# Optimization experiments

Hardware: AMD Instinct MI355X
Metric: run time of the kernel (lower is better)

The kernel has to match this reference:

```python
import jax, jax.numpy as jnp
import numpy as np

N, H, M, B = 512, 64, 1024, 256
ETA = 1.0
INIT_STD = 0.01

def setup_inputs() -> dict:
    key = jax.random.key(0)
    k1, k2, k3, k4 = jax.random.split(key, 4)
    # Binary +/-1 sequences and memory (as produced upstream in the repo)
    sequences = jnp.where(jax.random.uniform(k1, (B, N)) < 0.5, -1.0, 1.0).astype(jnp.float32)
    memory = jnp.where(jax.random.uniform(k2, (M, N)) < 0.5, -1.0, 1.0).astype(jnp.float32)
    A_logits = (INIT_STD * jax.random.normal(k3, (N, H, N))).astype(jnp.float32)
    B_logits = (INIT_STD * jax.random.normal(k4, (H, N))).astype(jnp.float32)
    return {"sequences": sequences, "memory": memory, "A_logits": A_logits, "B_logits": B_logits}

def reference(sequences, memory, A_logits, B_logits):
    # Vectorized version of DAM.train_batch's loss over positions n=1..N-1.
    n_dim = sequences.shape[1]
    # Causal mask: row for position n attends to indices i < n. Rows n=1..N-1.
    ns = jnp.arange(1, n_dim)[:, None, None]            # (N-1,1,1)
    idx = jnp.arange(n_dim)[None, None, :]              # (1,1,N)
    mask = idx < ns                                      # (N-1,1,N)
    neg_inf = jnp.asarray(-jnp.inf, A_logits.dtype)
    A = jax.nn.softmax(jnp.where(mask, A_logits[1:], neg_inf), axis=-1)  # (N-1,H,N), zeros outside mask
    Bn = jax.nn.softmax(B_logits, axis=-1)               # (H,N)
    phi_mu = jnp.einsum('hn,mn->mh', Bn, memory)         # (M,H) memory keys
    hat_phi = jnp.einsum('bi,nhi->bnh', sequences, A)    # (B,N-1,H) queries for every position at once
    score = ETA * jnp.einsum('bnh,mh->bnm', hat_phi, phi_mu)  # (B,N-1,M)
    pi = jax.nn.softmax(score, axis=-1)                  # retrieval distribution over memories
    plus = (memory[:, 1:] > 0).astype(pi.dtype)          # (M,N-1): memory bit at position n is +1
    prob = jnp.einsum('bnm,mn->bn', pi, plus)            # P(next bit = +1)
    prob = jnp.clip(prob, 1e-6, 1.0 - 1e-6)
    target = (sequences[:, 1:] > 0).astype(prob.dtype)
    bce = -(target * jnp.log(prob) + (1.0 - target) * jnp.log1p(-prob))
    # mean over batch per position, summed over positions, / (N-1) == global mean
    return jnp.mean(bce)
```

## Files before the change

kernel.cpp:

```cpp
#include <hip/hip_runtime.h>
#include <stdint.h>

#define NPOS 512
#define NH   64
#define NM   1024
#define NB   256
#define NM1  511

typedef __attribute__((ext_vector_type(8)))  short bf16x8;
typedef __attribute__((ext_vector_type(16))) float f32x16;
typedef __attribute__((ext_vector_type(4)))  float f32x4;
typedef __attribute__((ext_vector_type(4)))  int   i32x4;

#if __has_builtin(__builtin_amdgcn_exp2f)
#define EXP2F(x) __builtin_amdgcn_exp2f(x)
#else
#define EXP2F(x) __expf((x) * 0.69314718055994531f)
#endif

__device__ __forceinline__ unsigned short f2bf(float x) {
    unsigned u = __float_as_uint(x);
    u = (u + 0x7FFFu + ((u >> 16) & 1u)) >> 16;
    return (unsigned short)u;
}
__device__ __forceinline__ int pack2(unsigned short a, unsigned short b) {
    return (int)a | ((int)b << 16);
}

__global__ __launch_bounds__(256, 4)
void kA_prep(const float* __restrict__ seq, const float* __restrict__ Bl,
             const float* __restrict__ mem,
             unsigned short* __restrict__ seq_bf, float* __restrict__ BnT,
             float* __restrict__ plusT, float* __restrict__ out) {
    const int bid = blockIdx.x, t = threadIdx.x;
    if (bid < 128) {
        if (bid == 0 && t == 0) out[0] = 0.f;
        int idx = (bid * 256 + t) * 4;
        f32x4 v = *(const f32x4*)(seq + idx);
        int2 o;
        o.x = pack2(f2bf(v.x), f2bf(v.y));
        o.y = pack2(f2bf(v.z), f2bf(v.w));
        *(int2*)(seq_bf + idx) = o;
    } else if (bid < 144) {
        const int h = (bid - 128) * 4 + (t >> 6), l = t & 63;
        float v[8]; float mx = -1e30f;
#pragma unroll
        for (int j = 0; j < 8; j++) { v[j] = Bl[h * NPOS + l + 64 * j]; mx = fmaxf(mx, v[j]); }
#pragma unroll
        for (int o = 32; o; o >>= 1) mx = fmaxf(mx, __shfl_xor(mx, o));
        float s = 0.f;
#pragma unroll
        for (int j = 0; j < 8; j++) { v[j] = __expf(v[j] - mx); s += v[j]; }
#pragma unroll
        for (int o = 32; o; o >>= 1) s += __shfl_xor(s, o);
        float r = 1.0f / s;
#pragma unroll
        for (int j = 0; j < 8; j++) BnT[(l + 64 * j) * NH + h] = v[j] * r;
    } else {
        __shared__ float sT[64][65];
        const int bb = bid - 144;
        const int mt = bb >> 3, nt = bb & 7;
        const int rr = t >> 2, cc = t & 3;
        const float* src = mem + (size_t)(mt * 64 + rr) * NPOS + nt * 64 + cc * 16;
#pragma unroll
        for (int j = 0; j < 4; j++) {
            f32x4 v = *(const f32x4*)(src + j * 4);
            sT[rr][cc * 16 + j * 4 + 0] = (v.x > 0.f) ? 1.f : 0.f;
            sT[rr][cc * 16 + j * 4 + 1] = (v.y > 0.f) ? 1.f : 0.f;
            sT[rr][cc * 16 + j * 4 + 2] = (v.z > 0.f) ? 1.f : 0.f;
            sT[rr][cc * 16 + j * 4 + 3] = (v.w > 0.f) ? 1.f : 0.f;
        }
        __syncthreads();
        float* dst = plusT + (size_t)(nt * 64 + rr) * NM + mt * 64 + cc * 16;
#pragma unroll
        for (int j = 0; j < 4; j++) {
            f32x4 o;
            o.x = sT[cc * 16 + j * 4 + 0][rr];
            o.y = sT[cc * 16 + j * 4 + 1][rr];
            o.z = sT[cc * 16 + j * 4 + 2][rr];
            o.w = sT[cc * 16 + j * 4 + 3][rr];
            *(f32x4*)(dst + j * 4) = o;
        }
    }
}

__global__ __launch_bounds__(256, 4)
void k1b_phimu(const float* __restrict__ BnT, const float* __restrict__ mem,
               unsigned short* __restrict__ phimu) {
    const int m0 = blockIdx.x * 2, t = threadIdx.x;
    __shared__ float mrow[2][NPOS];
    __shared__ float part[2][256];
    {
        int row = t >> 7, c = (t & 127) * 4;
        *(f32x4*)(&mrow[row][c]) = *(const f32x4*)(mem + (size_t)(m0 + row) * NPOS + c);
    }
    __syncthreads();
    const int h = t & 63, seg = t >> 6;
    float a[2] = {0.f, 0.f};
    float b2[2] = {0.f, 0.f};
    const float* bp = BnT + seg * 128 * NH + h;
#pragma unroll 8
    for (int nn = 0; nn < 128; nn += 2) {
        float x0 = bp[nn * NH], x1 = bp[(nn + 1) * NH];
#pragma unroll
        for (int row = 0; row < 2; row++) {
            a[row]  = fmaf(x0, mrow[row][seg * 128 + nn], a[row]);
            b2[row] = fmaf(x1, mrow[row][seg * 128 + nn + 1], b2[row]);
        }
    }
#pragma unroll
    for (int row = 0; row < 2; row++) part[row][t] = a[row] + b2[row];
    __syncthreads();
    if (t < 64) {
#pragma unroll
        for (int row = 0; row < 2; row++) {
            float s = (part[row][t] + part[row][t + 64]) + (part[row][t + 128] + part[row][t + 192]);
            phimu[(m0 + row) * NH + t] = f2bf(s * 1.4426950408889634f);
        }
    }
}

__device__ __forceinline__ void p2_load(bf16x8 (&p)[4], const unsigned short* __restrict__ phimu,
                                        int tile, int r, int half) {
#pragma unroll
    for (int kq = 0; kq < 4; kq++)
        p[kq] = *(const bf16x8*)(phimu + (size_t)(tile * 32 + r) * NH + kq * 16 + half * 8);
}
__device__ __forceinline__ void p2_mfma(const bf16x8 (&p)[4], const bf16x8 (&q0)[4], const bf16x8 (&q1)[4],
                                        f32x16& a0, f32x16& a1) {
#pragma unroll
    for (int i = 0; i < 16; i++) { a0[i] = 0.f; a1[i] = 0.f; }
#pragma unroll
    for (int kq = 0; kq < 4; kq++) {
        a0 = __builtin_amdgcn_mfma_f32_32x32x16_bf16(p[kq], q0[kq], a0, 0, 0, 0);
        a1 = __builtin_amdgcn_mfma_f32_32x32x16_bf16(p[kq], q1[kq], a1, 0, 0, 0);
    }
}
__device__ __forceinline__ void p2_expsum(const f32x16& a0, const f32x16& a1, const float* s_plus,
                                          int mb, int half,
                                          f32x4& den0, f32x4& num0, f32x4& den1, f32x4& num1) {
#pragma unroll
    for (int g = 0; g < 4; g++) {
        f32x4 pv = *(const f32x4*)(s_plus + mb + 4 * half + 8 * g);
        f32x4 e0, e1;
#pragma unroll
        for (int j = 0; j < 4; j++) {
            e0[j] = EXP2F(a0[4 * g + j]);
            e1[j] = EXP2F(a1[4 * g + j]);
        }
        den0 += e0; num0 += e0 * pv;
        den1 += e1; num1 += e1 * pv;
    }
}

__global__ __launch_bounds__(256, 2)
void k23_fused(const float* __restrict__ Al, const unsigned short* __restrict__ seq_bf,
               const unsigned short* __restrict__ phimu, const float* __restrict__ plusT,
               const float* __restrict__ seq, float* __restrict__ out) {
    __shared__ __align__(16) unsigned short e_lds[2][64 * 72];
    __shared__ __align__(16) unsigned short q_lds[256 * 72];
    __shared__ float z_lds[64];
    __shared__ float s_plus[NM];

    const int t = threadIdx.x;
    const int n = NM1 - (int)blockIdx.x;
    const int ksteps = (n + 63) >> 6;
    const int wv = t >> 6, lane = t & 63, half = lane >> 5, r = lane & 31;

    if (t < 64) z_lds[t] = 0.f;
    *(f32x4*)(s_plus + t * 4) = *(const f32x4*)(plusT + (size_t)n * NM + t * 4);

    const int eh = t >> 2, ei = (t & 3) * 16;
    const float* arow = Al + ((size_t)n * NH + eh) * NPOS + ei;
    const unsigned short* s0 = seq_bf + (size_t)(wv * 64 + r) * NPOS;
    const unsigned short* s1 = seq_bf + (size_t)(wv * 64 + 32 + r) * NPOS;

    f32x16 acc00, acc01, acc10, acc11;
#pragma unroll
    for (int i = 0; i < 16; i++) { acc00[i] = 0.f; acc01[i] = 0.f; acc10[i] = 0.f; acc11[i] = 0.f; }

    f32x4 ea[4];
    bf16x8 sc0[4], sc1[4], sn0[4], sn1[4];
#pragma unroll
    for (int g = 0; g < 4; g++) ea[g] = *(const f32x4*)(arow + g * 4);
#pragma unroll
    for (int kq = 0; kq < 4; kq++) {
        sc0[kq] = *(const bf16x8*)(s0 + kq * 16 + half * 8);
        sc1[kq] = *(const bf16x8*)(s1 + kq * 16 + half * 8);
    }
    __syncthreads();

    for (int kk = 0; kk < ksteps; kk++) {
        const int k0 = kk * 64;
        unsigned short* ebuf = e_lds[kk & 1];
        {
            float zp = 0.f;
            unsigned short* ep = ebuf + eh * 72 + ei;
#pragma unroll
            for (int g = 0; g < 4; g++) {
                int i0 = k0 + ei + g * 4;
                float e0 = (i0 + 0 < n) ? __expf(ea[g].x) : 0.f;
                float e1 = (i0 + 1 < n) ? __expf(ea[g].y) : 0.f;
                float e2 = (i0 + 2 < n) ? __expf(ea[g].z) : 0.f;
                float e3 = (i0 + 3 < n) ? __expf(ea[g].w) : 0.f;
                zp += (e0 + e1) + (e2 + e3);
                int2 o; o.x = pack2(f2bf(e0), f2bf(e1)); o.y = pack2(f2bf(e2), f2bf(e3));
                *(int2*)(ep + g * 4) = o;
            }
            zp += __shfl_xor(zp, 1);
            zp += __shfl_xor(zp, 2);
            if ((t & 3) == 0) z_lds[eh] += zp;
        }
        if (kk + 1 < ksteps) {
#pragma unroll
            for (int g = 0; g < 4; g++) ea[g] = *(const f32x4*)(arow + k0 + 64 + g * 4);
#pragma unroll
            for (int kq = 0; kq < 4; kq++) {
                sn0[kq] = *(const bf16x8*)(s0 + k0 + 64 + kq * 16 + half * 8);
                sn1[kq] = *(const bf16x8*)(s1 + k0 + 64 + kq * 16 + half * 8);
            }
        }
        asm volatile("s_waitcnt lgkmcnt(0)" ::: "memory");
        __builtin_amdgcn_s_barrier();
        asm volatile("" ::: "memory");
        {
            const unsigned short* sB0 = ebuf + r * 72;
            const unsigned short* sB1 = sB0 + 32 * 72;
#pragma unroll
            for (int kq = 0; kq < 4; kq++) {
                const int ko = kq * 16 + half * 8;
                bf16x8 B0 = *(const bf16x8*)(sB0 + ko);
                bf16x8 B1 = *(const bf16x8*)(sB1 + ko);
                acc00 = __builtin_amdgcn_mfma_f32_32x32x16_bf16(sc0[kq], B0, acc00, 0, 0, 0);
                acc01 = __builtin_amdgcn_mfma_f32_32x32x16_bf16(sc0[kq], B1, acc01, 0, 0, 0);
                acc10 = __builtin_amdgcn_mfma_f32_32x32x16_bf16(sc1[kq], B0, acc10, 0, 0, 0);
                acc11 = __builtin_amdgcn_mfma_f32_32x32x16_bf16(sc1[kq], B1, acc11, 0, 0, 0);
            }
        }
        if (kk + 1 < ksteps) {
#pragma unroll
            for (int kq = 0; kq < 4; kq++) { sc0[kq] = sn0[kq]; sc1[kq] = sn1[kq]; }
        }
    }
    {
        float rz0 = 1.0f / z_lds[r];
        float rz1 = 1.0f / z_lds[32 + r];
#pragma unroll
        for (int reg = 0; reg < 16; reg++) {
            int row = (reg & 3) + 8 * (reg >> 2) + 4 * half;
            q_lds[(wv * 64 + row) * 72 + r]            = f2bf(acc00[reg] * rz0);
            q_lds[(wv * 64 + row) * 72 + 32 + r]       = f2bf(acc01[reg] * rz1);
            q_lds[(wv * 64 + 32 + row) * 72 + r]       = f2bf(acc10[reg] * rz0);
            q_lds[(wv * 64 + 32 + row) * 72 + 32 + r]  = f2bf(acc11[reg] * rz1);
        }
    }

    bf16x8 pA[4], pB[4];
    p2_load(pA, phimu, 0, r, half);
    p2_load(pB, phimu, 1, r, half);
    bf16x8 q0[4], q1[4];
#pragma unroll
    for (int kq = 0; kq < 4; kq++) {
        q0[kq] = *(const bf16x8*)(q_lds + (wv * 64 + r) * 72 + kq * 16 + half * 8);
        q1[kq] = *(const bf16x8*)(q_lds + (wv * 64 + 32 + r) * 72 + kq * 16 + half * 8);
    }

    f32x4 den0 = {0.f,0.f,0.f,0.f}, num0 = {0.f,0.f,0.f,0.f};
    f32x4 den1 = {0.f,0.f,0.f,0.f}, num1 = {0.f,0.f,0.f,0.f};
    f32x16 aA0, aA1, aB0, aB1;

    p2_mfma(pA, q0, q1, aA0, aA1);
    for (int it = 0; it < 32; it += 2) {
        if (it + 2 < 32) p2_load(pA, phimu, it + 2, r, half);
        p2_mfma(pB, q0, q1, aB0, aB1);
        if (it + 3 < 32) p2_load(pB, phimu, it + 3, r, half);
        p2_expsum(aA0, aA1, s_plus, it * 32, half, den0, num0, den1, num1);
        if (it + 2 < 32) p2_mfma(pA, q0, q1, aA0, aA1);
        p2_expsum(aB0, aB1, s_plus, (it + 1) * 32, half, den0, num0, den1, num1);
    }

    float d0 = (den0[0] + den0[1]) + (den0[2] + den0[3]);
    float nu0 = (num0[0] + num0[1]) + (num0[2] + num0[3]);
    float d1 = (den1[0] + den1[1]) + (den1[2] + den1[3]);
    float nu1 = (num1[0] + num1[1]) + (num1[2] + num1[3]);
    d0 += __shfl_xor(d0, 32); nu0 += __shfl_xor(nu0, 32);
    d1 += __shfl_xor(d1, 32); nu1 += __shfl_xor(nu1, 32);

    float* dsum = (float*)e_lds;
    float* nsum = dsum + 256;
    if (half == 0) {
        dsum[wv * 64 + r]      = d0; nsum[wv * 64 + r]      = nu0;
        dsum[wv * 64 + 32 + r] = d1; nsum[wv * 64 + 32 + r] = nu1;
    }
    __syncthreads();
    {
        float dd = dsum[t], nn = nsum[t];
        float p2 = nn / dd;
        p2 = fminf(fmaxf(p2, 1e-6f), 1.0f - 1e-6f);
        float tg = seq[(size_t)t * NPOS + n];
        float bce = (tg > 0.f) ? -logf(p2) : -logf(1.0f - p2);
#pragma unroll
        for (int o = 32; o; o >>= 1) bce += __shfl_xor(bce, o);
        if (lane == 0) z_lds[wv] = bce;
    }
    __syncthreads();
    if (t == 0)
        atomicAdd(out, (z_lds[0] + z_lds[1] + z_lds[2] + z_lds[3]) * (1.0f / 130816.0f));
}

extern "C" void kernel_launch(void* const* d_in, const int* in_sizes, int n_in,
                              void* d_out, int out_size, void* d_ws, size_t ws_size,
                              hipStream_t stream) {
    const float* seq = (const float*)d_in[0];
    const float* mem = (const float*)d_in[1];
    const float* Al  = (const float*)d_in[2];
    const float* Bl  = (const float*)d_in[3];

    char* ws = (char*)d_ws;
    unsigned short* seq_bf = (unsigned short*)(ws + 0);
    float*          BnT    = (float*)(ws + 262144);
    unsigned short* phimu  = (unsigned short*)(ws + 393216);
    float*          plusT  = (float*)(ws + 524288);
    float*          outp   = (float*)d_out;

    kA_prep<<<272, 256, 0, stream>>>(seq, Bl, mem, seq_bf, BnT, plusT, outp);
    k1b_phimu<<<512, 256, 0, stream>>>(BnT, mem, phimu);
    k23_fused<<<511, 256, 0, stream>>>(Al, seq_bf, phimu, plusT, seq, outp);
}
```

Measured before the change: 148.4 us.

## Compute softmax denominator and numerator via MFMA with bf16 exp weights

The exp-weighted sums over memories (denominator and plus-weighted numerator) are now computed with MFMA. Exponentials are packed to bf16 with v_cvt_pk_bf16_f32 and multiplied against a B operand whose lane 0 holds ones and lane 1 holds the plus bits. phimu is stored pre-swizzled into the MFMA fragment layout so the loads are contiguous, and k1b processes 8 memory rows per block. This removes the VALU accumulation and the s_plus LDS reads, but rounds the exp values to bf16, which reduces accuracy, and wastes most of the MFMA output columns.

New measurement: 142.1 us. -4.2%, faster.

```diff
diff --git a/kernel.cpp b/kernel.cpp
--- a/kernel.cpp
+++ b/kernel.cpp
@@ -25,6 +25,11 @@
 }
 __device__ __forceinline__ int pack2(unsigned short a, unsigned short b) {
     return (int)a | ((int)b << 16);
+}
+__device__ __forceinline__ int cvtpk(float lo, float hi) {
+    int r;
+    asm volatile("v_cvt_pk_bf16_f32 %0, %1, %2" : "=v"(r) : "v"(lo), "v"(hi));
+    return r;
 }
 
 __global__ __launch_bounds__(256, 4)
@@ -86,81 +91,63 @@
 
 __global__ __launch_bounds__(256, 4)
 void k1b_phimu(const float* __restrict__ BnT, const float* __restrict__ mem,
-               unsigned short* __restrict__ phimu) {
-    const int m0 = blockIdx.x * 2, t = threadIdx.x;
-    __shared__ float mrow[2][NPOS];
-    __shared__ float part[2][256];
-    {
-        int row = t >> 7, c = (t & 127) * 4;
-        *(f32x4*)(&mrow[row][c]) = *(const f32x4*)(mem + (size_t)(m0 + row) * NPOS + c);
+               unsigned short* __restrict__ phimuF) {
+    const int m0 = blockIdx.x * 8, t = threadIdx.x;
+    __shared__ float mrow[8][NPOS];
+    __shared__ float part[8][256];
+#pragma unroll
+    for (int ch = 0; ch < 4; ch++) {
+        int idx = ch * 256 + t;
+        int row = idx >> 7, col = (idx & 127) * 4;
+        *(f32x4*)(&mrow[row][col]) = *(const f32x4*)(mem + (size_t)(m0 + row) * NPOS + col);
     }
     __syncthreads();
     const int h = t & 63, seg = t >> 6;
-    float a[2] = {0.f, 0.f};
-    float b2[2] = {0.f, 0.f};
+    float a[8], b2[8];
+#pragma unroll
+    for (int row = 0; row < 8; row++) { a[row] = 0.f; b2[row] = 0.f; }
     const float* bp = BnT + seg * 128 * NH + h;
-#pragma unroll 8
+#pragma unroll 4
     for (int nn = 0; nn < 128; nn += 2) {
         float x0 = bp[nn * NH], x1 = bp[(nn + 1) * NH];
 #pragma unroll
-        for (int row = 0; row < 2; row++) {
+        for (int row = 0; row < 8; row++) {
             a[row]  = fmaf(x0, mrow[row][seg * 128 + nn], a[row]);
             b2[row] = fmaf(x1, mrow[row][seg * 128 + nn + 1], b2[row]);
         }
     }
 #pragma unroll
-    for (int row = 0; row < 2; row++) part[row][t] = a[row] + b2[row];
+    for (int row = 0; row < 8; row++) part[row][t] = a[row] + b2[row];
     __syncthreads();
     if (t < 64) {
 #pragma unroll
-        for (int row = 0; row < 2; row++) {
+        for (int row = 0; row < 8; row++) {
             float s = (part[row][t] + part[row][t + 64]) + (part[row][t + 128] + part[row][t + 192]);
-            phimu[(m0 + row) * NH + t] = f2bf(s * 1.4426950408889634f);
-        }
-    }
-}
-
-__device__ __forceinline__ void p2_load(bf16x8 (&p)[4], const unsigned short* __restrict__ phimu,
-                                        int tile, int r, int half) {
+            unsigned short v = f2bf(s * 1.4426950408889634f);
+            const int m = m0 + row;
+            const int tile = m >> 5, rr = m & 31;
+            const int kq = t >> 4, hi2 = (t >> 3) & 1, j = t & 7;
+            phimuF[(size_t)((tile * 4 + kq) * 64 + rr + 32 * hi2) * 8 + j] = v;
+        }
+    }
+}
+
+__device__ __forceinline__ void p2_loadF(bf16x8 (&p)[4], const unsigned short* __restrict__ phimuF,
+                                         int tile, int lane) {
 #pragma unroll
     for (int kq = 0; kq < 4; kq++)
-        p[kq] = *(const bf16x8*)(phimu + (size_t)(tile * 32 + r) * NH + kq * 16 + half * 8);
-}
-__device__ __forceinline__ void p2_mfma(const bf16x8 (&p)[4], const bf16x8 (&q0)[4], const bf16x8 (&q1)[4],
-                                        f32x16& a0, f32x16& a1) {
-#pragma unroll
-    for (int i = 0; i < 16; i++) { a0[i] = 0.f; a1[i] = 0.f; }
-#pragma unroll
-    for (int kq = 0; kq < 4; kq++) {
-        a0 = __builtin_amdgcn_mfma_f32_32x32x16_bf16(p[kq], q0[kq], a0, 0, 0, 0);
-        a1 = __builtin_amdgcn_mfma_f32_32x32x16_bf16(p[kq], q1[kq], a1, 0, 0, 0);
-    }
-}
-__device__ __forceinline__ void p2_expsum(const f32x16& a0, const f32x16& a1, const float* s_plus,
-                                          int mb, int half,
-                                          f32x4& den0, f32x4& num0, f32x4& den1, f32x4& num1) {
-#pragma unroll
-    for (int g = 0; g < 4; g++) {
-        f32x4 pv = *(const f32x4*)(s_plus + mb + 4 * half + 8 * g);
-        f32x4 e0, e1;
-#pragma unroll
-        for (int j = 0; j < 4; j++) {
-            e0[j] = EXP2F(a0[4 * g + j]);
-            e1[j] = EXP2F(a1[4 * g + j]);
-        }
-        den0 += e0; num0 += e0 * pv;
-        den1 += e1; num1 += e1 * pv;
-    }
+        p[kq] = *(const bf16x8*)(phimuF + (size_t)((tile * 4 + kq) * 64 + lane) * 8);
 }
 
 __global__ __launch_bounds__(256, 2)
 void k23_fused(const float* __restrict__ Al, const unsigned short* __restrict__ seq_bf,
-               const unsigned short* __restrict__ phimu, const float* __restrict__ plusT,
+               const unsigned short* __restrict__ phimuF, const float* __restrict__ plusT,
                const float* __restrict__ seq, float* __restrict__ out) {
     __shared__ __align__(16) unsigned short e_lds[2][64 * 72];
     __shared__ __align__(16) unsigned short q_lds[256 * 72];
+    __shared__ __align__(16) unsigned short plusbf[32 * 2 * 2 * 8];
     __shared__ float z_lds[64];
-    __shared__ float s_plus[NM];
+    __shared__ float w_lds[4];
 
     const int t = threadIdx.x;
     const int n = NM1 - (int)blockIdx.x;
@@ -168,7 +155,15 @@
     const int wv = t >> 6, lane = t & 63, half = lane >> 5, r = lane & 31;
 
     if (t < 64) z_lds[t] = 0.f;
-    *(f32x4*)(s_plus + t * 4) = *(const f32x4*)(plusT + (size_t)n * NM + t * 4);
+    if (t < 128) {
+        const int tile = t >> 2, mm = (t >> 1) & 1, hh = t & 1;
+        const float* src = plusT + (size_t)n * NM + tile * 32 + mm * 16 + hh * 4;
+        f32x4 v0 = *(const f32x4*)(src);
+        f32x4 v1 = *(const f32x4*)(src + 8);
+        unsigned short* dst = plusbf + (size_t)((tile * 2 + mm) * 2 + hh) * 8;
+        dst[0] = f2bf(v0.x); dst[1] = f2bf(v0.y); dst[2] = f2bf(v0.z); dst[3] = f2bf(v0.w);
+        dst[4] = f2bf(v1.x); dst[5] = f2bf(v1.y); dst[6] = f2bf(v1.z); dst[7] = f2bf(v1.w);
+    }
 
     const int eh = t >> 2, ei = (t & 3) * 16;
     const float* arow = Al + ((size_t)n * NH + eh) * NPOS + ei;
@@ -192,7 +187,7 @@
 
     for (int kk = 0; kk < ksteps; kk++) {
         const int k0 = kk * 64;
-        unsigned short* ebuf = e_lds[kk & 1];
+        unsigned short* ebuf = (unsigned short*)e_lds[kk & 1];
         {
             float zp = 0.f;
             unsigned short* ep = ebuf + eh * 72 + ei;
@@ -255,42 +250,77 @@
         }
     }
 
-    bf16x8 pA[4], pB[4];
-    p2_load(pA, phimu, 0, r, half);
-    p2_load(pB, phimu, 1, r, half);
+    bf16x8 p[4], pn[4];
+    p2_loadF(p, phimuF, 0, lane);
     bf16x8 q0[4], q1[4];
 #pragma unroll
     for (int kq = 0; kq < 4; kq++) {
         q0[kq] = *(const bf16x8*)(q_lds + (wv * 64 + r) * 72 + kq * 16 + half * 8);
         q1[kq] = *(const bf16x8*)(q_lds + (wv * 64 + 32 + r) * 72 + kq * 16 + half * 8);
     }
-
-    f32x4 den0 = {0.f,0.f,0.f,0.f}, num0 = {0.f,0.f,0.f,0.f};
-    f32x4 den1 = {0.f,0.f,0.f,0.f}, num1 = {0.f,0.f,0.f,0.f};
-    f32x16 aA0, aA1, aB0, aB1;
-
-    p2_mfma(pA, q0, q1, aA0, aA1);
-    for (int it = 0; it < 32; it += 2) {
-        if (it + 2 < 32) p2_load(pA, phimu, it + 2, r, half);
-        p2_mfma(pB, q0, q1, aB0, aB1);
-        if (it + 3 < 32) p2_load(pB, phimu, it + 3, r, half);
-        p2_expsum(aA0, aA1, s_plus, it * 32, half, den0, num0, den1, num1);
-        if (it + 2 < 32) p2_mfma(pA, q0, q1, aA0, aA1);
-        p2_expsum(aB0, aB1, s_plus, (it + 1) * 32, half, den0, num0, den1, num1);
-    }
-
-    float d0 = (den0[0] + den0[1]) + (den0[2] + den0[3]);
-    float nu0 = (num0[0] + num0[1]) + (num0[2] + num0[3]);
-    float d1 = (den1[0] + den1[1]) + (den1[2] + den1[3]);
-    float nu1 = (num1[0] + num1[1]) + (num1[2] + num1[3]);
-    d0 += __shfl_xor(d0, 32); nu0 += __shfl_xor(nu0, 32);
-    d1 += __shfl_xor(d1, 32); nu1 += __shfl_xor(nu1, 32);
-
+    f32x16 zacc, accD0, accD1;
+#pragma unroll
+    for (int i = 0; i < 16; i++) { zacc[i] = 0.f; accD0[i] = 0.f; accD1[i] = 0.f; }
+
+    const unsigned onespat = (r == 0) ? 0x3F803F80u : 0u;
+    const unsigned pmask   = (r == 1) ? 0xFFFFFFFFu : 0u;
+
+    for (int it = 0; it < 32; ++it) {
+        if (it < 31) p2_loadF(pn, phimuF, it + 1, lane);
+        f32x16 a0, a1;
+        a0 = __builtin_amdgcn_mfma_f32_32x32x16_bf16(p[0], q0[0], zacc, 0, 0, 0);
+        a1 = __builtin_amdgcn_mfma_f32_32x32x16_bf16(p[0], q1[0], zacc, 0, 0, 0);
+#pragma unroll
+        for (int kq = 1; kq < 4; kq++) {
+            a0 = __builtin_amdgcn_mfma_f32_32x32x16_bf16(p[kq], q0[kq], a0, 0, 0, 0);
+            a1 = __builtin_amdgcn_mfma_f32_32x32x16_bf16(p[kq], q1[kq], a1, 0, 0, 0);
+        }
+        i32x4 w1r = *(const i32x4*)(plusbf + (size_t)(4 * it + half) * 8);
+        i32x4 w2r = *(const i32x4*)(plusbf + (size_t)(4 * it + 2 + half) * 8);
+        i32x4 W1, W2;
+        W1.x = onespat | (w1r.x & pmask); W1.y = onespat | (w1r.y & pmask);
+        W1.z = onespat | (w1r.z & pmask); W1.w = onespat | (w1r.w & pmask);
+        W2.x = onespat | (w2r.x & pmask); W2.y = onespat | (w2r.y & pmask);
+        W2.z = onespat | (w2r.z & pmask); W2.w = onespat | (w2r.w & pmask);
+        {
+            float e00 = EXP2F(a0[0]),  e01 = EXP2F(a0[1]),  e02 = EXP2F(a0[2]),  e03 = EXP2F(a0[3]);
+            float e04 = EXP2F(a0[4]),  e05 = EXP2F(a0[5]),  e06 = EXP2F(a0[6]),  e07 = EXP2F(a0[7]);
+            float e08 = EXP2F(a0[8]),  e09 = EXP2F(a0[9]),  e10 = EXP2F(a0[10]), e11 = EXP2F(a0[11]);
+            float e12 = EXP2F(a0[12]), e13 = EXP2F(a0[13]), e14 = EXP2F(a0[14]), e15 = EXP2F(a0[15]);
+            i32x4 A1, A2;
+            A1.x = cvtpk(e00, e01); A1.y = cvtpk(e02, e03); A1.z = cvtpk(e04, e05); A1.w = cvtpk(e06, e07);
+            A2.x = cvtpk(e08, e09); A2.y = cvtpk(e10, e11); A2.z = cvtpk(e12, e13); A2.w = cvtpk(e14, e15);
+            accD0 = __builtin_amdgcn_mfma_f32_32x32x16_bf16(*(bf16x8*)&A1, *(bf16x8*)&W1, accD0, 0, 0, 0);
+            accD0 = __builtin_amdgcn_mfma_f32_32x32x16_bf16(*(bf16x8*)&A2, *(bf16x8*)&W2, accD0, 0, 0, 0);
+        }
+        {
+            float e00 = EXP2F(a1[0]),  e01 = EXP2F(a1[1]),  e02 = EXP2F(a1[2]),  e03 = EXP2F(a1[3]);
+            float e04 = EXP2F(a1[4]),  e05 = EXP2F(a1[5]),  e06 = EXP2F(a1[6]),  e07 = EXP2F(a1[7]);
+            float e08 = EXP2F(a1[8]),  e09 = EXP2F(a1[9]),  e10 = EXP2F(a1[10]), e11 = EXP2F(a1[11]);
+            float e12 = EXP2F(a1[12]), e13 = EXP2F(a1[13]), e14 = EXP2F(a1[14]), e15 = EXP2F(a1[15]);
+            i32x4 A1, A2;
+            A1.x = cvtpk(e00, e01); A1.y = cvtpk(e02, e03); A1.z = cvtpk(e04, e05); A1.w = cvtpk(e06, e07);
+            A2.x = cvtpk(e08, e09); A2.y = cvtpk(e10, e11); A2.z = cvtpk(e12, e13); A2.w = cvtpk(e14, e15);
+            accD1 = __builtin_amdgcn_mfma_f32_32x32x16_bf16(*(bf16x8*)&A1, *(bf16x8*)&W1, accD1, 0, 0, 0);
+            accD1 = __builtin_amdgcn_mfma_f32_32x32x16_bf16(*(bf16x8*)&A2, *(bf16x8*)&W2, accD1, 0, 0, 0);
+        }
+        if (it < 31) {
+#pragma unroll
+            for (int kq = 0; kq < 4; kq++) p[kq] = pn[kq];
+        }
+    }
+
+    __syncthreads();
     float* dsum = (float*)e_lds;
     float* nsum = dsum + 256;
-    if (half == 0) {
-        dsum[wv * 64 + r]      = d0; nsum[wv * 64 + r]      = nu0;
-        dsum[wv * 64 + 32 + r] = d1; nsum[wv * 64 + 32 + r] = nu1;
+    if (r < 2) {
+        float* dst = (r == 0) ? dsum : nsum;
+#pragma unroll
+        for (int reg = 0; reg < 16; reg++) {
+            int row = (reg & 3) + 8 * (reg >> 2) + 4 * half;
+            dst[wv * 64 + row]      = accD0[reg];
+            dst[wv * 64 + 32 + row] = accD1[reg];
+        }
     }
     __syncthreads();
     {
@@ -301,11 +331,11 @@
         float bce = (tg > 0.f) ? -logf(p2) : -logf(1.0f - p2);
 #pragma unroll
         for (int o = 32; o; o >>= 1) bce += __shfl_xor(bce, o);
-        if (lane == 0) z_lds[wv] = bce;
+        if (lane == 0) w_lds[wv] = bce;
     }
     __syncthreads();
     if (t == 0)
-        atomicAdd(out, (z_lds[0] + z_lds[1] + z_lds[2] + z_lds[3]) * (1.0f / 130816.0f));
+        atomicAdd(out, (w_lds[0] + w_lds[1] + w_lds[2] + w_lds[3]) * (1.0f / 130816.0f));
 }
 
 extern "C" void kernel_launch(void* const* d_in, const int* in_sizes, int n_in,
@@ -319,11 +349,11 @@
     char* ws = (char*)d_ws;
     unsigned short* seq_bf = (unsigned short*)(ws + 0);
     float*          BnT    = (float*)(ws + 262144);
-    unsigned short* phimu  = (unsigned short*)(ws + 393216);
+    unsigned short* phimuF = (unsigned short*)(ws + 393216);
     float*          plusT  = (float*)(ws + 524288);
     float*          outp   = (float*)d_out;
 
     kA_prep<<<272, 256, 0, stream>>>(seq, Bl, mem, seq_bf, BnT, plusT, outp);
-    k1b_phimu<<<512, 256, 0, stream>>>(BnT, mem, phimu);
-    k23_fused<<<511, 256, 0, stream>>>(Al, seq_bf, phimu, plusT, seq, outp);
-}
+    k1b_phimu<<<128, 256, 0, stream>>>(BnT, mem, phimuF);
+    k23_fused<<<511, 256, 0, stream>>>(Al, seq_bf, phimuF, plusT, seq, outp);
+}
```
